# Kernel optimization log

Measured on AMD Instinct MI355X. Metric: run time of the kernel, lower is better.

## Reference

```python
import jax, jax.numpy as jnp
import numpy as np

KS = 3   # kernel_size = sqrt(window_size=9)
PAD = 1  # KS // 2


def _unfold(t):
    # F.unfold(t, kernel_size=3, padding=1) then view(B,C,K,HW).permute(0,3,2,1)
    # -> (B, HW, K, C), K enumerated row-major over the 3x3 window.
    B, C, H, W = t.shape
    tp = jnp.pad(t, ((0, 0), (0, 0), (PAD, PAD), (PAD, PAD)))
    patches = jnp.stack(
        [tp[:, :, i:i + H, j:j + W] for i in range(KS) for j in range(KS)],
        axis=2,
    )  # (B, C, K, H, W)
    return patches.reshape(B, C, KS * KS, H * W).transpose(0, 3, 2, 1)


def setup_inputs() -> dict:
    key = jax.random.key(0)
    ks = jax.random.split(key, 8)
    B, C, H, W = 8, 256, 64, 64
    Cr = C // 8  # reduction=8
    return {
        "x": jax.random.normal(ks[0], (B, C, H, W), dtype=jnp.float32),
        "Wq": jax.random.normal(ks[1], (Cr, C), dtype=jnp.float32) * 0.02,
        "bq": jax.random.normal(ks[2], (Cr,), dtype=jnp.float32) * 0.02,
        "Wk": jax.random.normal(ks[3], (Cr, C), dtype=jnp.float32) * 0.02,
        "bk": jax.random.normal(ks[4], (Cr,), dtype=jnp.float32) * 0.02,
        "Wv": jax.random.normal(ks[5], (C, C), dtype=jnp.float32) * 0.02,
        "bv": jax.random.normal(ks[6], (C,), dtype=jnp.float32) * 0.02,
        "gamma": jax.random.normal(ks[7], (1,), dtype=jnp.float32) * 0.1,
    }


def reference(x, Wq, bq, Wk, bk, Wv, bv, gamma):
    B, C, H, W = x.shape
    # 1x1 convs == per-pixel linear projections
    q = jnp.einsum('bchw,oc->bohw', x, Wq) + bq[None, :, None, None]
    k = jnp.einsum('bchw,oc->bohw', x, Wk) + bk[None, :, None, None]
    v = jnp.einsum('bchw,oc->bohw', x, Wv) + bv[None, :, None, None]
    ku = _unfold(k)  # (B, HW, K, Cr)
    vu = _unfold(v)  # (B, HW, K, C)
    qf = q.reshape(B, -1, H * W).transpose(0, 2, 1)  # (B, HW, Cr)
    energy = jnp.einsum('bqc,bqkc->bqk', qf, ku)     # (B, HW, K)
    attn = jax.nn.softmax(energy, axis=-1)
    out = jnp.einsum('bqk,bqkc->bqc', attn, vu)      # (B, HW, C)
    out = out.transpose(0, 2, 1).reshape(B, C, H, W)
    return gamma * out + x
```

## Files before the change

### kernel.cpp

```cpp
#include <hip/hip_runtime.h>

#define HW   4096
#define HIMG 64
#define WIMG 64
#define CC   256
#define CR   32
#define B_   8

typedef __attribute__((ext_vector_type(8))) short bf16x8;
typedef __attribute__((ext_vector_type(4))) float f32x4;

__device__ inline unsigned short f2bf(float f) {
    union { float f; unsigned u; } v; v.f = f;
    return (unsigned short)((v.u + 0x8000u) >> 16);
}

__global__ __launch_bounds__(256) void wconv(
    const float* __restrict__ Wq, const float* __restrict__ bq,
    const float* __restrict__ Wk, const float* __restrict__ bk,
    const float* __restrict__ Wv, const float* __restrict__ bv,
    unsigned short* __restrict__ Wb, float* __restrict__ bb)
{
    const int o = blockIdx.x;
    const float* src; const float* bsrc; int orel;
    if (o < 32)      { src = Wq; bsrc = bq; orel = o;      }
    else if (o < 64) { src = Wk; bsrc = bk; orel = o - 32; }
    else             { src = Wv; bsrc = bv; orel = o - 64; }
    Wb[o * CC + threadIdx.x] = f2bf(src[orel * CC + threadIdx.x]);
    if (threadIdx.x == 0) bb[o] = bsrc[orel];
}

__global__ __launch_bounds__(256) void xconv(
    const float* __restrict__ x, unsigned short* __restrict__ xt)
{
    __shared__ unsigned short tile[64 * 72];
    const int b = blockIdx.z, c0 = blockIdx.y * 64, p0 = blockIdx.x * 64;
    const int t = threadIdx.x;

    #pragma unroll
    for (int i = 0; i < 4; ++i) {
        int idx = t + 256 * i;
        int c = idx >> 4, p4 = (idx & 15) * 4;
        float4 v = *(const float4*)&x[((size_t)b * CC + c0 + c) * HW + p0 + p4];
        tile[(p4 + 0) * 72 + c] = f2bf(v.x);
        tile[(p4 + 1) * 72 + c] = f2bf(v.y);
        tile[(p4 + 2) * 72 + c] = f2bf(v.z);
        tile[(p4 + 3) * 72 + c] = f2bf(v.w);
    }
    __syncthreads();
    #pragma unroll
    for (int i = 0; i < 2; ++i) {
        int chunk = t + 256 * i;
        int p = chunk >> 3, s8 = chunk & 7;
        uint4 u = *(const uint4*)&tile[p * 72 + s8 * 8];
        *(uint4*)&xt[((size_t)b * HW + p0 + p) * CC + c0 + s8 * 8] = u;
    }
}

__global__ __launch_bounds__(256) void proj_gemm(
    const unsigned short* __restrict__ Wb, const float* __restrict__ bb,
    const unsigned short* __restrict__ xt,
    float* __restrict__ q, float* __restrict__ k, float* __restrict__ vv)
{
    __shared__ unsigned short As[64 * 72];
    __shared__ unsigned short Bs[128 * 72];
    const int b   = blockIdx.z;
    const int o0  = blockIdx.y * 64;
    const int hw0 = blockIdx.x * 128;
    const int t    = threadIdx.x;
    const int lane = t & 63, wv = t >> 6;
    const int m16  = lane & 15, quad = lane >> 4;

    f32x4 acc[4][2];
    #pragma unroll
    for (int tm = 0; tm < 4; ++tm)
        #pragma unroll
        for (int tn = 0; tn < 2; ++tn)
            acc[tm][tn] = (f32x4){0.f, 0.f, 0.f, 0.f};

    for (int kc = 0; kc < 4; ++kc) {
        const int k0 = kc * 64;
        if (kc) __syncthreads();
        #pragma unroll
        for (int i = 0; i < 2; ++i) {
            int idx = t + 256 * i, row = idx >> 3, s8 = idx & 7;
            *(uint4*)&As[row * 72 + s8 * 8] =
                *(const uint4*)&Wb[(o0 + row) * CC + k0 + s8 * 8];
        }
        #pragma unroll
        for (int i = 0; i < 4; ++i) {
            int idx = t + 256 * i, row = idx >> 3, s8 = idx & 7;
            *(uint4*)&Bs[row * 72 + s8 * 8] =
                *(const uint4*)&xt[((size_t)b * HW + hw0 + row) * CC + k0 + s8 * 8];
        }
        __syncthreads();

        #pragma unroll
        for (int ks = 0; ks < 2; ++ks) {
            bf16x8 af[4], bf[2];
            #pragma unroll
            for (int tm = 0; tm < 4; ++tm)
                af[tm] = *(const bf16x8*)&As[(tm * 16 + m16) * 72 + ks * 32 + quad * 8];
            #pragma unroll
            for (int tn = 0; tn < 2; ++tn)
                bf[tn] = *(const bf16x8*)&Bs[(wv * 32 + tn * 16 + m16) * 72 + ks * 32 + quad * 8];
            #pragma unroll
            for (int tm = 0; tm < 4; ++tm)
                #pragma unroll
                for (int tn = 0; tn < 2; ++tn)
                    acc[tm][tn] = __builtin_amdgcn_mfma_f32_16x16x32_bf16(
                        af[tm], bf[tn], acc[tm][tn], 0, 0, 0);
        }
    }

    #pragma unroll
    for (int tm = 0; tm < 4; ++tm) {
        const int ob = o0 + tm * 16;
        float* dst; int orel, nch;
        if (ob < 32)      { dst = q;  orel = ob;      nch = CR; }
        else if (ob < 64) { dst = k;  orel = ob - 32; nch = CR; }
        else              { dst = vv; orel = ob - 64; nch = CC; }
        #pragma unroll
        for (int r = 0; r < 4; ++r) {
            const int orow = quad * 4 + r;
            const float bias = bb[ob + orow];
            const size_t rowbase = ((size_t)b * nch + orel + orow) * HW;
            #pragma unroll
            for (int tn = 0; tn < 2; ++tn) {
                int hw = hw0 + wv * 32 + tn * 16 + m16;
                dst[rowbase + hw] = acc[tm][tn][r] + bias;
            }
        }
    }
}

__global__ __launch_bounds__(256) void attn_w(
    const float* __restrict__ q_, const float* __restrict__ k_,
    float* __restrict__ aw)
{
    __shared__ float qs[64][33];
    __shared__ float ks[3][64][33];
    __shared__ float es[64][9];
    const int h = blockIdx.x, b = blockIdx.y, t = threadIdx.x;

    #pragma unroll
    for (int i = 0; i < 2; ++i) {
        int idx = t + 256 * i, cr = idx >> 4, p4 = (idx & 15) * 4;
        float4 vq = *(const float4*)&q_[((size_t)b * CR + cr) * HW + h * WIMG + p4];
        qs[p4 + 0][cr] = vq.x; qs[p4 + 1][cr] = vq.y;
        qs[p4 + 2][cr] = vq.z; qs[p4 + 3][cr] = vq.w;
    }
    #pragma unroll
    for (int r = 0; r < 3; ++r) {
        int hh = h + r - 1;
        bool ok = (hh >= 0) && (hh < HIMG);
        #pragma unroll
        for (int i = 0; i < 2; ++i) {
            int idx = t + 256 * i, cr = idx >> 4, p4 = (idx & 15) * 4;
            float4 vk = make_float4(0.f, 0.f, 0.f, 0.f);
            if (ok)
                vk = *(const float4*)&k_[((size_t)b * CR + cr) * HW + hh * WIMG + p4];
            ks[r][p4 + 0][cr] = vk.x; ks[r][p4 + 1][cr] = vk.y;
            ks[r][p4 + 2][cr] = vk.z; ks[r][p4 + 3][cr] = vk.w;
        }
    }
    __syncthreads();

    for (int id = t; id < 576; id += 256) {
        int px = id / 9, kk = id - px * 9;
        int di = kk / 3, dj = kk - di * 3;
        int hh = h + di - 1, ww = px + dj - 1;
        float e = 0.f;
        if (hh >= 0 && hh < HIMG && ww >= 0 && ww < WIMG) {
            float s = 0.f;
            #pragma unroll
            for (int c = 0; c < CR; ++c) s = fmaf(qs[px][c], ks[di][ww][c], s);
            e = s;
        }
        es[px][kk] = e;
    }
    __syncthreads();

    if (t < 64) {
        float m = es[t][0];
        #pragma unroll
        for (int kk = 1; kk < 9; ++kk) m = fmaxf(m, es[t][kk]);
        float ex[9]; float ssum = 0.f;
        #pragma unroll
        for (int kk = 0; kk < 9; ++kk) { ex[kk] = __expf(es[t][kk] - m); ssum += ex[kk]; }
        float inv = 1.f / ssum;
        float* dst = &aw[((size_t)b * HW + h * WIMG + t) * 12];
        #pragma unroll
        for (int kk = 0; kk < 9; ++kk) dst[kk] = ex[kk] * inv;
    }
}

__global__ __launch_bounds__(256) void apply(
    const float* __restrict__ x, const float* __restrict__ vv,
    const float* __restrict__ aw, const float* __restrict__ gamma,
    float* __restrict__ out)
{
    __shared__ float vs[3][32][72];
    __shared__ float aws[64][12];
    const int h = blockIdx.x, cb = blockIdx.y, b = blockIdx.z, t = threadIdx.x;

    if (t < 192) {
        int px = t / 3, seg = t - px * 3;
        *(float4*)&aws[px][seg * 4] =
            *(const float4*)&aw[((size_t)b * HW + h * WIMG + px) * 12 + seg * 4];
    }
    #pragma unroll
    for (int i = 0; i < 6; ++i) {
        int idx = t + 256 * i;
        int p4 = (idx & 15) * 4, c = (idx >> 4) & 31, r = idx >> 9;
        int hh = h + r - 1;
        float4 val = make_float4(0.f, 0.f, 0.f, 0.f);
        if (hh >= 0 && hh < HIMG)
            val = *(const float4*)&vv[((size_t)b * CC + cb * 32 + c) * HW + hh * WIMG + p4];
        *(float4*)&vs[r][c][4 + p4] = val;
    }
    if (t < 96) {
        int r = t >> 5, c = t & 31;
        float4 z = make_float4(0.f, 0.f, 0.f, 0.f);
        *(float4*)&vs[r][c][0]  = z;
        *(float4*)&vs[r][c][68] = z;
    }
    __syncthreads();

    const int px0 = (t & 15) * 4;
    const int cl  = t >> 4;
    float w[4][9];
    #pragma unroll
    for (int i = 0; i < 4; ++i)
        #pragma unroll
        for (int kk = 0; kk < 9; ++kk) w[i][kk] = aws[px0 + i][kk];
    const float g = gamma[0];

    #pragma unroll
    for (int ci = 0; ci < 2; ++ci) {
        int c = cl + 16 * ci;
        float a0 = 0.f, a1 = 0.f, a2 = 0.f, a3 = 0.f;
        #pragma unroll
        for (int r = 0; r < 3; ++r) {
            float4 ctr = *(float4*)&vs[r][c][4 + px0];
            float  lft = vs[r][c][3 + px0];
            float  rgt = vs[r][c][8 + px0];
            int r3 = r * 3;
            a0 = fmaf(w[0][r3], lft,   fmaf(w[0][r3+1], ctr.x, fmaf(w[0][r3+2], ctr.y, a0)));
            a1 = fmaf(w[1][r3], ctr.x, fmaf(w[1][r3+1], ctr.y, fmaf(w[1][r3+2], ctr.z, a1)));
            a2 = fmaf(w[2][r3], ctr.y, fmaf(w[2][r3+1], ctr.z, fmaf(w[2][r3+2], ctr.w, a2)));
            a3 = fmaf(w[3][r3], ctr.z, fmaf(w[3][r3+1], ctr.w, fmaf(w[3][r3+2], rgt,  a3)));
        }
        size_t base = ((size_t)b * CC + cb * 32 + c) * HW + h * WIMG + px0;
        float4 xa = *(const float4*)&x[base];
        float4 o;
        o.x = fmaf(g, a0, xa.x); o.y = fmaf(g, a1, xa.y);
        o.z = fmaf(g, a2, xa.z); o.w = fmaf(g, a3, xa.w);
        *(float4*)&out[base] = o;
    }
}

extern "C" void kernel_launch(void* const* d_in, const int* in_sizes, int n_in,
                              void* d_out, int out_size, void* d_ws, size_t ws_size,
                              hipStream_t stream)
{
    const float* x     = (const float*)d_in[0];
    const float* Wq    = (const float*)d_in[1];
    const float* bq    = (const float*)d_in[2];
    const float* Wk    = (const float*)d_in[3];
    const float* bk    = (const float*)d_in[4];
    const float* Wv    = (const float*)d_in[5];
    const float* bv    = (const float*)d_in[6];
    const float* gamma = (const float*)d_in[7];
    float* out = (float*)d_out;

    unsigned short* xt = (unsigned short*)d_ws;
    float* q  = (float*)((char*)d_ws + (size_t)B_ * HW * CC * 2);
    float* k  = q  + (size_t)B_ * CR * HW;
    float* v  = k  + (size_t)B_ * CR * HW;
    float* aw = v  + (size_t)B_ * CC * HW;
    unsigned short* Wb = (unsigned short*)(aw + (size_t)B_ * HW * 12);
    float* bb = (float*)(Wb + 320 * CC);

    wconv<<<dim3(320), 256, 0, stream>>>(Wq, bq, Wk, bk, Wv, bv, Wb, bb);
    xconv<<<dim3(HW / 64, CC / 64, B_), 256, 0, stream>>>(x, xt);
    proj_gemm<<<dim3(HW / 128, 320 / 64, B_), 256, 0, stream>>>(Wb, bb, xt, q, k, v);
    attn_w<<<dim3(HIMG, B_), 256, 0, stream>>>(q, k, aw);
    apply<<<dim3(HIMG, CC / 32, B_), 256, 0, stream>>>(x, v, aw, gamma, out);
}
```

Measured before the change: 146.8 us.

## Fuse x bf16 transpose into projection GEMM and store V as bf16

Removes the separate xconv kernel: the projection GEMM now reads fp32 x directly, transposes and converts it to bf16 in shared memory with an XOR swizzle. Each block now covers all 320 output channels for 64 pixels, so x is read once instead of once per output-channel tile. V is stored as bf16 and widened back in the apply kernel, halving the V write and read traffic. The cost is a large shared-memory footprint and heavier per-block work, which lowers occupancy, plus extra rounding of V.

```diff
diff --git a/kernel.cpp b/kernel.cpp
--- a/kernel.cpp
+++ b/kernel.cpp
@@ -13,6 +13,12 @@
 __device__ inline unsigned short f2bf(float f) {
     union { float f; unsigned u; } v; v.f = f;
     return (unsigned short)((v.u + 0x8000u) >> 16);
+}
+__device__ inline float bf2f(unsigned short h) {
+    union { unsigned u; float f; } v; v.u = ((unsigned)h) << 16; return v.f;
+}
+__device__ inline unsigned pack2(float a, float b) {
+    return (unsigned)f2bf(a) | ((unsigned)f2bf(b) << 16);
 }
 
 __global__ __launch_bounds__(256) void wconv(
@@ -30,105 +36,108 @@
     if (threadIdx.x == 0) bb[o] = bsrc[orel];
 }
 
-__global__ __launch_bounds__(256) void xconv(
-    const float* __restrict__ x, unsigned short* __restrict__ xt)
-{
-    __shared__ unsigned short tile[64 * 72];
-    const int b = blockIdx.z, c0 = blockIdx.y * 64, p0 = blockIdx.x * 64;
-    const int t = threadIdx.x;
-
-    #pragma unroll
-    for (int i = 0; i < 4; ++i) {
-        int idx = t + 256 * i;
-        int c = idx >> 4, p4 = (idx & 15) * 4;
-        float4 v = *(const float4*)&x[((size_t)b * CC + c0 + c) * HW + p0 + p4];
-        tile[(p4 + 0) * 72 + c] = f2bf(v.x);
-        tile[(p4 + 1) * 72 + c] = f2bf(v.y);
-        tile[(p4 + 2) * 72 + c] = f2bf(v.z);
-        tile[(p4 + 3) * 72 + c] = f2bf(v.w);
-    }
-    __syncthreads();
-    #pragma unroll
-    for (int i = 0; i < 2; ++i) {
-        int chunk = t + 256 * i;
-        int p = chunk >> 3, s8 = chunk & 7;
-        uint4 u = *(const uint4*)&tile[p * 72 + s8 * 8];
-        *(uint4*)&xt[((size_t)b * HW + p0 + p) * CC + c0 + s8 * 8] = u;
-    }
-}
-
 __global__ __launch_bounds__(256) void proj_gemm(
     const unsigned short* __restrict__ Wb, const float* __restrict__ bb,
-    const unsigned short* __restrict__ xt,
-    float* __restrict__ q, float* __restrict__ k, float* __restrict__ vv)
-{
-    __shared__ unsigned short As[64 * 72];
-    __shared__ unsigned short Bs[128 * 72];
-    const int b   = blockIdx.z;
-    const int o0  = blockIdx.y * 64;
-    const int hw0 = blockIdx.x * 128;
+    const float* __restrict__ x,
+    float* __restrict__ q, float* __restrict__ k,
+    unsigned short* __restrict__ vv)
+{
+    __shared__ unsigned short As[320 * 72];
+    __shared__ float          xt32[64 * 65];
+    __shared__ unsigned short Bs[64 * 64];
+
+    const int b   = blockIdx.y;
+    const int hw0 = blockIdx.x * 64;
     const int t    = threadIdx.x;
     const int lane = t & 63, wv = t >> 6;
     const int m16  = lane & 15, quad = lane >> 4;
 
-    f32x4 acc[4][2];
-    #pragma unroll
-    for (int tm = 0; tm < 4; ++tm)
-        #pragma unroll
-        for (int tn = 0; tn < 2; ++tn)
-            acc[tm][tn] = (f32x4){0.f, 0.f, 0.f, 0.f};
+    f32x4 acc[5][4];
+    #pragma unroll
+    for (int i = 0; i < 5; ++i)
+        #pragma unroll
+        for (int n = 0; n < 4; ++n)
+            acc[i][n] = (f32x4){0.f, 0.f, 0.f, 0.f};
 
     for (int kc = 0; kc < 4; ++kc) {
         const int k0 = kc * 64;
         if (kc) __syncthreads();
-        #pragma unroll
-        for (int i = 0; i < 2; ++i) {
-            int idx = t + 256 * i, row = idx >> 3, s8 = idx & 7;
+
+        #pragma unroll
+        for (int i = 0; i < 10; ++i) {
+            int idx = t + 256 * i;
+            int row = idx >> 3, s8 = idx & 7;
             *(uint4*)&As[row * 72 + s8 * 8] =
-                *(const uint4*)&Wb[(o0 + row) * CC + k0 + s8 * 8];
+                *(const uint4*)&Wb[row * CC + k0 + s8 * 8];
         }
         #pragma unroll
         for (int i = 0; i < 4; ++i) {
-            int idx = t + 256 * i, row = idx >> 3, s8 = idx & 7;
-            *(uint4*)&Bs[row * 72 + s8 * 8] =
-                *(const uint4*)&xt[((size_t)b * HW + hw0 + row) * CC + k0 + s8 * 8];
+            int idx = t + 256 * i;
+            int c = idx >> 4, p4 = (idx & 15) * 4;
+            float4 vx = *(const float4*)&x[((size_t)b * CC + k0 + c) * HW + hw0 + p4];
+            *(float4*)&xt32[c * 65 + p4] = vx;
         }
         __syncthreads();
 
+        {
+            const int px = lane;
+            const int c0 = wv * 16;
+            float f[16];
+            #pragma unroll
+            for (int j = 0; j < 16; ++j)
+                f[j] = xt32[(c0 + j) * 65 + px];
+            uint4 w0, w1;
+            w0.x = pack2(f[0],  f[1]);  w0.y = pack2(f[2],  f[3]);
+            w0.z = pack2(f[4],  f[5]);  w0.w = pack2(f[6],  f[7]);
+            w1.x = pack2(f[8],  f[9]);  w1.y = pack2(f[10], f[11]);
+            w1.z = pack2(f[12], f[13]); w1.w = pack2(f[14], f[15]);
+            const int lg0 = c0 >> 3, sw = px & 7;
+            *(uint4*)&Bs[px * 64 + ((lg0     ^ sw) * 8)] = w0;
+            *(uint4*)&Bs[px * 64 + (((lg0+1) ^ sw) * 8)] = w1;
+        }
+        __syncthreads();
+
         #pragma unroll
         for (int ks = 0; ks < 2; ++ks) {
-            bf16x8 af[4], bf[2];
-            #pragma unroll
-            for (int tm = 0; tm < 4; ++tm)
-                af[tm] = *(const bf16x8*)&As[(tm * 16 + m16) * 72 + ks * 32 + quad * 8];
-            #pragma unroll
-            for (int tn = 0; tn < 2; ++tn)
-                bf[tn] = *(const bf16x8*)&Bs[(wv * 32 + tn * 16 + m16) * 72 + ks * 32 + quad * 8];
-            #pragma unroll
-            for (int tm = 0; tm < 4; ++tm)
+            bf16x8 af[5], bf[4];
+            #pragma unroll
+            for (int i = 0; i < 5; ++i)
+                af[i] = *(const bf16x8*)&As[((wv * 5 + i) * 16 + m16) * 72
+                                            + ks * 32 + quad * 8];
+            #pragma unroll
+            for (int n = 0; n < 4; ++n) {
+                int px = n * 16 + m16;
+                int lg = ks * 4 + quad;
+                bf[n] = *(const bf16x8*)&Bs[px * 64 + ((lg ^ (px & 7)) * 8)];
+            }
+            #pragma unroll
+            for (int i = 0; i < 5; ++i)
                 #pragma unroll
-                for (int tn = 0; tn < 2; ++tn)
-                    acc[tm][tn] = __builtin_amdgcn_mfma_f32_16x16x32_bf16(
-                        af[tm], bf[tn], acc[tm][tn], 0, 0, 0);
-        }
-    }
-
-    #pragma unroll
-    for (int tm = 0; tm < 4; ++tm) {
-        const int ob = o0 + tm * 16;
-        float* dst; int orel, nch;
-        if (ob < 32)      { dst = q;  orel = ob;      nch = CR; }
-        else if (ob < 64) { dst = k;  orel = ob - 32; nch = CR; }
-        else              { dst = vv; orel = ob - 64; nch = CC; }
+                for (int n = 0; n < 4; ++n)
+                    acc[i][n] = __builtin_amdgcn_mfma_f32_16x16x32_bf16(
+                        af[i], bf[n], acc[i][n], 0, 0, 0);
+        }
+    }
+
+    #pragma unroll
+    for (int i = 0; i < 5; ++i) {
+        const int ob = (wv * 5 + i) * 16;
         #pragma unroll
         for (int r = 0; r < 4; ++r) {
             const int orow = quad * 4 + r;
             const float bias = bb[ob + orow];
-            const size_t rowbase = ((size_t)b * nch + orel + orow) * HW;
-            #pragma unroll
-            for (int tn = 0; tn < 2; ++tn) {
-                int hw = hw0 + wv * 32 + tn * 16 + m16;
-                dst[rowbase + hw] = acc[tm][tn][r] + bias;
+            if (ob < 64) {
+                float* dst = (ob < 32) ? q : k;
+                int orel = (ob < 32) ? ob : ob - 32;
+                size_t rowbase = ((size_t)b * CR + orel + orow) * HW;
+                #pragma unroll
+                for (int n = 0; n < 4; ++n)
+                    dst[rowbase + hw0 + n * 16 + m16] = acc[i][n][r] + bias;
+            } else {
+                size_t rowbase = ((size_t)b * CC + (ob - 64) + orow) * HW;
+                #pragma unroll
+                for (int n = 0; n < 4; ++n)
+                    vv[rowbase + hw0 + n * 16 + m16] = f2bf(acc[i][n][r] + bias);
             }
         }
     }
@@ -196,7 +205,7 @@
 }
 
 __global__ __launch_bounds__(256) void apply(
-    const float* __restrict__ x, const float* __restrict__ vv,
+    const float* __restrict__ x, const unsigned short* __restrict__ vv,
     const float* __restrict__ aw, const float* __restrict__ gamma,
     float* __restrict__ out)
 {
@@ -215,8 +224,11 @@
         int p4 = (idx & 15) * 4, c = (idx >> 4) & 31, r = idx >> 9;
         int hh = h + r - 1;
         float4 val = make_float4(0.f, 0.f, 0.f, 0.f);
-        if (hh >= 0 && hh < HIMG)
-            val = *(const float4*)&vv[((size_t)b * CC + cb * 32 + c) * HW + hh * WIMG + p4];
+        if (hh >= 0 && hh < HIMG) {
+            ushort4 u = *(const ushort4*)&vv[((size_t)b * CC + cb * 32 + c) * HW
+                                             + hh * WIMG + p4];
+            val = make_float4(bf2f(u.x), bf2f(u.y), bf2f(u.z), bf2f(u.w));
+        }
         *(float4*)&vs[r][c][4 + p4] = val;
     }
     if (t < 96) {
@@ -274,17 +286,15 @@
     const float* gamma = (const float*)d_in[7];
     float* out = (float*)d_out;
 
-    unsigned short* xt = (unsigned short*)d_ws;
-    float* q  = (float*)((char*)d_ws + (size_t)B_ * HW * CC * 2);
-    float* k  = q  + (size_t)B_ * CR * HW;
-    float* v  = k  + (size_t)B_ * CR * HW;
-    float* aw = v  + (size_t)B_ * CC * HW;
+    float* q  = (float*)d_ws;
+    float* k  = q + (size_t)B_ * CR * HW;
+    unsigned short* vv = (unsigned short*)(k + (size_t)B_ * CR * HW);
+    float* aw = (float*)(vv + (size_t)B_ * CC * HW);
     unsigned short* Wb = (unsigned short*)(aw + (size_t)B_ * HW * 12);
     float* bb = (float*)(Wb + 320 * CC);
 
     wconv<<<dim3(320), 256, 0, stream>>>(Wq, bq, Wk, bk, Wv, bv, Wb, bb);
-    xconv<<<dim3(HW / 64, CC / 64, B_), 256, 0, stream>>>(x, xt);
-    proj_gemm<<<dim3(HW / 128, 320 / 64, B_), 256, 0, stream>>>(Wb, bb, xt, q, k, v);
+    proj_gemm<<<dim3(HW / 64, B_), 256, 0, stream>>>(Wb, bb, x, q, k, vv);
     attn_w<<<dim3(HIMG, B_), 256, 0, stream>>>(q, k, aw);
-    apply<<<dim3(HIMG, CC / 32, B_), 256, 0, stream>>>(x, v, aw, gamma, out);
-}
+    apply<<<dim3(HIMG, CC / 32, B_), 256, 0, stream>>>(x, vv, aw, gamma, out);
+}
```

New measurement: 134.1 us. -8.6%, faster.
